# Optimization experiments

Measured on AMD Instinct MI355X. Metric: run time of the kernel, lower is better.

## Reference

```python
import jax, jax.numpy as jnp
import numpy as np
from jax.scipy.linalg import expm

N = 2048
B = 16384
S = 0.1  # Euler step size s


def _A_hat(Theta):
    # row-softmax of Theta
    A = jax.nn.softmax(Theta, axis=1)
    # zero_diag=True path: mask diagonal, renormalize rows (guard empty rows)
    mask = 1.0 - jnp.eye(N, dtype=Theta.dtype)
    A = A * mask
    rs = jnp.sum(A, axis=1, keepdims=True)
    rs = jnp.where(rs > 0, rs, jnp.ones_like(rs))
    return A / rs


def setup_inputs() -> dict:
    key = jax.random.key(0)
    k1, k2 = jax.random.split(key)
    x = jax.random.normal(k1, (B, N), dtype=jnp.float32)
    # kaiming_uniform_(a=0) on [N,N]: bound = sqrt(6 / N)
    bound = float(np.sqrt(6.0 / N))
    Theta = jax.random.uniform(k2, (N, N), dtype=jnp.float32, minval=-bound, maxval=bound)
    return {"x": x, "Theta": Theta}


def reference(x, Theta):
    A = _A_hat(Theta)
    L = jnp.eye(N, dtype=Theta.dtype) - A          # normalized Laplacian
    M = expm(-S * L)                               # scaling-and-squaring matrix exp
    return x @ M.T                                 # [B, N]
```

## Files before the change

### kernel.cpp

```cpp
#include <hip/hip_runtime.h>
#include <hip/hip_bf16.h>
#include <cstdint>
#include <cstddef>

typedef unsigned short u16;
typedef unsigned int u32;
typedef __attribute__((ext_vector_type(8))) short bf16x8;
typedef __attribute__((ext_vector_type(4))) float f32x4;

#define ND 2048
#define BD 16384

#define C0 0.9048374180359595f
#define C1 0.09048374180359595f
#define C2 0.004524187090179798f
#define C3 1.5080623633932658e-4f
#define C4 3.770155908483165e-6f

__device__ __forceinline__ u16 f2bf(float f) {
  union { float f; u32 u; } v; v.f = f;
  u32 x = v.u;
  return (u16)((x + 0x7fffu + ((x >> 16) & 1u)) >> 16);
}

__device__ __forceinline__ float bf2f(u16 b) {
  union { u32 u; float f; } v; v.u = ((u32)b) << 16; return v.f;
}

__device__ __forceinline__ void cp16(const void* g, void* l) {
  __builtin_amdgcn_global_load_lds(
      (const __attribute__((address_space(1))) u32*)g,
      (__attribute__((address_space(3))) u32*)l, 16, 0, 0);
}

__global__ void cvt_x(const float* __restrict__ in, u16* __restrict__ out) {
  const size_t i = ((size_t)blockIdx.x * 256 + threadIdx.x) * 8;
  float4 a = ((const float4*)(in + i))[0];
  float4 b = ((const float4*)(in + i))[1];
  union { u16 u[8]; uint4 v; } o;
  o.u[0] = f2bf(a.x); o.u[1] = f2bf(a.y); o.u[2] = f2bf(a.z); o.u[3] = f2bf(a.w);
  o.u[4] = f2bf(b.x); o.u[5] = f2bf(b.y); o.u[6] = f2bf(b.z); o.u[7] = f2bf(b.w);
  *((uint4*)(out + i)) = o.v;
}

__global__ void row_softmax(const float* __restrict__ Theta, u16* __restrict__ Abf) {
  const int row = blockIdx.x;
  const int t = threadIdx.x;
  const float* tr = Theta + (size_t)row * ND;
  const int j0 = t * 8;
  float4 v0 = ((const float4*)tr)[t * 2];
  float4 v1 = ((const float4*)tr)[t * 2 + 1];
  float vals[8] = {v0.x, v0.y, v0.z, v0.w, v1.x, v1.y, v1.z, v1.w};

  float mx = -1e30f;
#pragma unroll
  for (int j = 0; j < 8; ++j)
    if (j0 + j != row) mx = fmaxf(mx, vals[j]);
#pragma unroll
  for (int o = 32; o > 0; o >>= 1) mx = fmaxf(mx, __shfl_xor(mx, o, 64));

  __shared__ float redm[4], reds[4];
  const int wv = t >> 6, ln = t & 63;
  if (ln == 0) redm[wv] = mx;
  __syncthreads();
  mx = fmaxf(fmaxf(redm[0], redm[1]), fmaxf(redm[2], redm[3]));

  float e[8];
  float s = 0.f;
#pragma unroll
  for (int j = 0; j < 8; ++j) {
    e[j] = (j0 + j == row) ? 0.f : expf(vals[j] - mx);
    s += e[j];
  }
#pragma unroll
  for (int o = 32; o > 0; o >>= 1) s += __shfl_xor(s, o, 64);
  if (ln == 0) reds[wv] = s;
  __syncthreads();
  s = reds[0] + reds[1] + reds[2] + reds[3];
  const float inv = 1.0f / s;

  union { u16 u[8]; uint4 v; } ab;
#pragma unroll
  for (int j = 0; j < 8; ++j) ab.u[j] = f2bf(e[j] * inv);
  *((uint4*)(Abf + (size_t)row * ND + j0)) = ab.v;
}

__global__ void transpose_bf16(const u16* __restrict__ in, u16* __restrict__ out) {
  __shared__ u16 tile[64][65];
  const int bx = blockIdx.x & 31, by = blockIdx.x >> 5;
  const int x = threadIdx.x & 63, y0 = threadIdx.x >> 6;
#pragma unroll
  for (int yy = y0; yy < 64; yy += 4)
    tile[yy][x] = in[(size_t)(by * 64 + yy) * ND + bx * 64 + x];
  __syncthreads();
#pragma unroll
  for (int yy = y0; yy < 64; yy += 4)
    out[(size_t)(bx * 64 + yy) * ND + by * 64 + x] = tile[x][yy];
}

template <int BM, int BN, int WM, int WN, int THREADS, int MODE>
__global__ __launch_bounds__(THREADS, 2) void gemm_deep(
    const u16* __restrict__ Ag, const u16* __restrict__ Bg,
    float* __restrict__ Fo, u16* __restrict__ Bo, u16* __restrict__ Bo2,
    const u16* __restrict__ Aux, const float* __restrict__ Xf,
    int Nn, int K, int gridn) {
  constexpr int LOGM = (BM == 256) ? 8 : 7;
  constexpr int LOGN = (BN == 256) ? 8 : 7;
  constexpr int FM = BM / WM / 16;
  constexpr int FN = BN / WN / 16;
  constexpr int CHA = BM * 4 / THREADS;
  constexpr int CHB = BN * 4 / THREADS;

  __shared__ u16 lA[3][BM * 32];
  __shared__ u16 lB[3][BN * 32];

  const int tid = threadIdx.x;
  const int lane = tid & 63;
  const int wave = tid >> 6;
  const int wm = wave / WN;
  const int wn = wave % WN;
  const int lr = lane & 15;
  const int kc = lane >> 4;

  const int nwg = gridDim.x;
  const int bid = blockIdx.x;
  const int swz = (bid & 7) * (nwg >> 3) + (bid >> 3);
  const int bm = swz / gridn;
  const int bn = swz % gridn;

  const u16* Abase = Ag + (size_t)bm * BM * K;
  const u16* Bbase = Bg + (size_t)bn * BN * K;

  f32x4 acc[FM][FN];
#pragma unroll
  for (int i = 0; i < FM; ++i)
#pragma unroll
    for (int j = 0; j < FN; ++j)
      acc[i][j] = (f32x4){0.f, 0.f, 0.f, 0.f};

  auto stage = [&](int s, int kt) {
    const int kbase = kt * 32;
#pragma unroll
    for (int q = 0; q < CHA; ++q) {
      int c = q * THREADS + tid;
      int kcc = c >> LOGM, row = c & (BM - 1);
      cp16(Abase + (size_t)row * K + kbase + kcc * 8, &lA[s][c * 8]);
    }
#pragma unroll
    for (int q = 0; q < CHB; ++q) {
      int c = q * THREADS + tid;
      int kcc = c >> LOGN, col = c & (BN - 1);
      cp16(Bbase + (size_t)col * K + kbase + kcc * 8, &lB[s][c * 8]);
    }
  };

  auto compute = [&](int s) {
    bf16x8 af[FM], bg[FN];
#pragma unroll
    for (int m = 0; m < FM; ++m) {
      int row = wm * (BM / WM) + m * 16 + lr;
      af[m] = *(const bf16x8*)&lA[s][(kc * BM + row) * 8];
    }
#pragma unroll
    for (int n = 0; n < FN; ++n) {
      int col = wn * (BN / WN) + n * 16 + lr;
      bg[n] = *(const bf16x8*)&lB[s][(kc * BN + col) * 8];
    }
    __builtin_amdgcn_s_setprio(1);
#pragma unroll
    for (int m = 0; m < FM; ++m)
#pragma unroll
      for (int n = 0; n < FN; ++n)
        acc[m][n] = __builtin_amdgcn_mfma_f32_16x16x32_bf16(af[m], bg[n], acc[m][n], 0, 0, 0);
    __builtin_amdgcn_s_setprio(0);
  };

  const int NT = K >> 5;
  stage(0, 0);
  stage(1, 1);
  for (int t = 0; t < NT - 2; ++t) {
    stage((t + 2) % 3, t + 2);
    asm volatile("s_waitcnt vmcnt(8)" ::: "memory");
    __builtin_amdgcn_s_barrier();
    compute(t % 3);
    __builtin_amdgcn_s_barrier();
  }
  asm volatile("s_waitcnt vmcnt(4)" ::: "memory");
  __builtin_amdgcn_s_barrier();
  compute((NT - 2) % 3);
  __builtin_amdgcn_s_barrier();
  asm volatile("s_waitcnt vmcnt(0)" ::: "memory");
  __builtin_amdgcn_s_barrier();
  compute((NT - 1) % 3);

  const int r0 = (lane >> 4) << 2;
#pragma unroll
  for (int m = 0; m < FM; ++m) {
    const int grow0 = bm * BM + wm * (BM / WM) + m * 16 + r0;
#pragma unroll
    for (int n = 0; n < FN; ++n) {
      const int gcol = bn * BN + wn * (BN / WN) + n * 16 + lr;
#pragma unroll
      for (int r = 0; r < 4; ++r) {
        const int grow = grow0 + r;
        const size_t idx = (size_t)grow * Nn + gcol;
        const float v = acc[m][n][r];
        if (MODE == 3) {
          Bo[idx] = f2bf(v);
          float tv = ((grow == gcol) ? C2 : 0.0f) + C3 * bf2f(Aux[idx]) + C4 * v;
          Bo2[idx] = f2bf(tv);
        } else if (MODE == 1) {
          Bo[idx] = f2bf(C1 * bf2f(Aux[idx]) + v);
        } else {
          Fo[idx] = C0 * Xf[idx] + v;
        }
      }
    }
  }
}

extern "C" void kernel_launch(void* const* d_in, const int* in_sizes, int n_in,
                              void* d_out, int out_size, void* d_ws, size_t ws_size,
                              hipStream_t stream) {
  const float* x = (const float*)d_in[0];
  const float* Theta = (const float*)d_in[1];
  float* out = (float*)d_out;

  char* ws = (char*)d_ws;
  u16* xbf  = (u16*)(ws);
  u16* Abf  = (u16*)(ws + 67108864);
  u16* Atbf = (u16*)(ws + 75497472);
  u16* P2   = (u16*)(ws + 83886080);
  u16* Tbf  = (u16*)(ws + 92274688);
  u16* Ttbf = (u16*)(ws + 100663296);
  u16* Rbf  = (u16*)(ws + 109051904);

  cvt_x<<<dim3(16384), dim3(256), 0, stream>>>(x, xbf);
  row_softmax<<<dim3(2048), dim3(256), 0, stream>>>(Theta, Abf);
  transpose_bf16<<<dim3(1024), dim3(256), 0, stream>>>(Abf, Atbf);
  gemm_deep<128, 128, 2, 2, 256, 3><<<dim3(256), dim3(256), 0, stream>>>(
      Abf, Atbf, nullptr, P2, Tbf, Abf, nullptr, ND, ND, 16);
  transpose_bf16<<<dim3(1024), dim3(256), 0, stream>>>(Tbf, Ttbf);
  gemm_deep<128, 128, 2, 2, 256, 1><<<dim3(256), dim3(256), 0, stream>>>(
      P2, Ttbf, nullptr, Rbf, nullptr, Abf, nullptr, ND, ND, 16);
  gemm_deep<256, 256, 2, 4, 512, 2><<<dim3(512), dim3(512), 0, stream>>>(
      xbf, Rbf, out, nullptr, nullptr, nullptr, x, ND, ND, 8);
}
```

Baseline: 635.6 us.

## Rewrite GEMM as half-tile ping-pong pipeline with BK=64 double buffering

Replaces the three-stage BK=32 GEMM with a double-buffered BK=64 kernel. Each block tile is split into four quadrant sub-tiles, and their LDS reads, MFMAs and next-tile prefetches are interleaved with barriers between them. The small 2048x2048 GEMMs switch from 128x128 tiles on 256 blocks to 64x64 tiles with 128 threads on 1024 blocks, to fill more compute units. Tile mapping changes to column-major block order (swz % gridm). The intent is better overlap of global loads with MFMA and higher occupancy, at the cost of more barriers and a more fragile hand-counted vmcnt schedule.

```diff
diff --git a/kernel.cpp b/kernel.cpp
--- a/kernel.cpp
+++ b/kernel.cpp
@@ -99,124 +99,148 @@
 }
 
 template <int BM, int BN, int WM, int WN, int THREADS, int MODE>
-__global__ __launch_bounds__(THREADS, 2) void gemm_deep(
+__global__ __launch_bounds__(THREADS, 2) void gemm8(
     const u16* __restrict__ Ag, const u16* __restrict__ Bg,
     float* __restrict__ Fo, u16* __restrict__ Bo, u16* __restrict__ Bo2,
     const u16* __restrict__ Aux, const float* __restrict__ Xf,
-    int Nn, int K, int gridn) {
-  constexpr int LOGM = (BM == 256) ? 8 : 7;
-  constexpr int LOGN = (BN == 256) ? 8 : 7;
-  constexpr int FM = BM / WM / 16;
-  constexpr int FN = BN / WN / 16;
-  constexpr int CHA = BM * 4 / THREADS;
-  constexpr int CHB = BN * 4 / THREADS;
-
-  __shared__ u16 lA[3][BM * 32];
-  __shared__ u16 lB[3][BN * 32];
+    int Nn, int K, int gridm) {
+  constexpr int BK = 64;
+  constexpr int HM = BM / 2, HN = BN / 2;
+  constexpr int RH = HM / WM, CH = HN / WN;
+  constexpr int FMH = RH / 16, FNH = CH / 16;
+  constexpr int LA = HM * 8 / THREADS;
+  constexpr int LB = HN * 8 / THREADS;
+  static_assert(LA == 2 && LB == 2, "vmcnt(4) math assumes 2+2 loads per half-pair");
+  static_assert(FMH >= 1 && FNH >= 1, "bad wave geometry");
+
+  __shared__ u16 lA[2][2][HM * BK];
+  __shared__ u16 lB[2][2][HN * BK];
 
   const int tid = threadIdx.x;
   const int lane = tid & 63;
   const int wave = tid >> 6;
-  const int wm = wave / WN;
-  const int wn = wave % WN;
-  const int lr = lane & 15;
-  const int kc = lane >> 4;
-
-  const int nwg = gridDim.x;
-  const int bid = blockIdx.x;
+  const int wm = wave / WN, wn = wave % WN;
+  const int lr = lane & 15, khi = lane >> 4;
+
+  const int nwg = gridDim.x, bid = blockIdx.x;
   const int swz = (bid & 7) * (nwg >> 3) + (bid >> 3);
-  const int bm = swz / gridn;
-  const int bn = swz % gridn;
-
-  const u16* Abase = Ag + (size_t)bm * BM * K;
-  const u16* Bbase = Bg + (size_t)bn * BN * K;
-
-  f32x4 acc[FM][FN];
-#pragma unroll
-  for (int i = 0; i < FM; ++i)
-#pragma unroll
-    for (int j = 0; j < FN; ++j)
+  const int bm = swz % gridm, bn = swz / gridm;
+
+  const u16* Ab = Ag + (size_t)bm * BM * K;
+  const u16* Bb = Bg + (size_t)bn * BN * K;
+
+  f32x4 acc[2 * FMH][2 * FNH];
+#pragma unroll
+  for (int i = 0; i < 2 * FMH; ++i)
+#pragma unroll
+    for (int j = 0; j < 2 * FNH; ++j)
       acc[i][j] = (f32x4){0.f, 0.f, 0.f, 0.f};
 
-  auto stage = [&](int s, int kt) {
-    const int kbase = kt * 32;
-#pragma unroll
-    for (int q = 0; q < CHA; ++q) {
+  auto stA = [&](int b, int h, int kt) {
+#pragma unroll
+    for (int q = 0; q < LA; ++q) {
       int c = q * THREADS + tid;
-      int kcc = c >> LOGM, row = c & (BM - 1);
-      cp16(Abase + (size_t)row * K + kbase + kcc * 8, &lA[s][c * 8]);
+      int kc = c / HM, row = c % HM;
+      cp16(Ab + (size_t)(h * HM + row) * K + kt * BK + kc * 8, &lA[b][h][c * 8]);
     }
-#pragma unroll
-    for (int q = 0; q < CHB; ++q) {
+  };
+  auto stB = [&](int b, int h, int kt) {
+#pragma unroll
+    for (int q = 0; q < LB; ++q) {
       int c = q * THREADS + tid;
-      int kcc = c >> LOGN, col = c & (BN - 1);
-      cp16(Bbase + (size_t)col * K + kbase + kcc * 8, &lB[s][c * 8]);
+      int kc = c / HN, col = c % HN;
+      cp16(Bb + (size_t)(h * HN + col) * K + kt * BK + kc * 8, &lB[b][h][c * 8]);
     }
   };
 
-  auto compute = [&](int s) {
-    bf16x8 af[FM], bg[FN];
-#pragma unroll
-    for (int m = 0; m < FM; ++m) {
-      int row = wm * (BM / WM) + m * 16 + lr;
-      af[m] = *(const bf16x8*)&lA[s][(kc * BM + row) * 8];
-    }
-#pragma unroll
-    for (int n = 0; n < FN; ++n) {
-      int col = wn * (BN / WN) + n * 16 + lr;
-      bg[n] = *(const bf16x8*)&lB[s][(kc * BN + col) * 8];
-    }
+  bf16x8 af[FMH][2], bfr[FNH][2];
+  auto rdA = [&](int b, int mh) {
+#pragma unroll
+    for (int fm = 0; fm < FMH; ++fm)
+#pragma unroll
+      for (int ks = 0; ks < 2; ++ks) {
+        int row = wm * RH + fm * 16 + lr;
+        int kc = ks * 4 + khi;
+        af[fm][ks] = *(const bf16x8*)&lA[b][mh][(kc * HM + row) * 8];
+      }
+  };
+  auto rdB = [&](int b, int nh) {
+#pragma unroll
+    for (int fn = 0; fn < FNH; ++fn)
+#pragma unroll
+      for (int ks = 0; ks < 2; ++ks) {
+        int col = wn * CH + fn * 16 + lr;
+        int kc = ks * 4 + khi;
+        bfr[fn][ks] = *(const bf16x8*)&lB[b][nh][(kc * HN + col) * 8];
+      }
+  };
+  auto mm = [&](int mh, int nh) {
     __builtin_amdgcn_s_setprio(1);
 #pragma unroll
-    for (int m = 0; m < FM; ++m)
-#pragma unroll
-      for (int n = 0; n < FN; ++n)
-        acc[m][n] = __builtin_amdgcn_mfma_f32_16x16x32_bf16(af[m], bg[n], acc[m][n], 0, 0, 0);
+    for (int ks = 0; ks < 2; ++ks)
+#pragma unroll
+      for (int fm = 0; fm < FMH; ++fm)
+#pragma unroll
+        for (int fn = 0; fn < FNH; ++fn)
+          acc[mh * FMH + fm][nh * FNH + fn] = __builtin_amdgcn_mfma_f32_16x16x32_bf16(
+              af[fm][ks], bfr[fn][ks], acc[mh * FMH + fm][nh * FNH + fn], 0, 0, 0);
     __builtin_amdgcn_s_setprio(0);
   };
 
-  const int NT = K >> 5;
-  stage(0, 0);
-  stage(1, 1);
-  for (int t = 0; t < NT - 2; ++t) {
-    stage((t + 2) % 3, t + 2);
-    asm volatile("s_waitcnt vmcnt(8)" ::: "memory");
-    __builtin_amdgcn_s_barrier();
-    compute(t % 3);
-    __builtin_amdgcn_s_barrier();
-  }
+  const int NT = K / BK;
+  stA(0, 0, 0); stB(0, 0, 0); stB(0, 1, 0); stA(0, 1, 0);
   asm volatile("s_waitcnt vmcnt(4)" ::: "memory");
   __builtin_amdgcn_s_barrier();
-  compute((NT - 2) % 3);
-  __builtin_amdgcn_s_barrier();
-  asm volatile("s_waitcnt vmcnt(0)" ::: "memory");
-  __builtin_amdgcn_s_barrier();
-  compute((NT - 1) % 3);
-
-  const int r0 = (lane >> 4) << 2;
-#pragma unroll
-  for (int m = 0; m < FM; ++m) {
-    const int grow0 = bm * BM + wm * (BM / WM) + m * 16 + r0;
-#pragma unroll
-    for (int n = 0; n < FN; ++n) {
-      const int gcol = bn * BN + wn * (BN / WN) + n * 16 + lr;
-#pragma unroll
-      for (int r = 0; r < 4; ++r) {
-        const int grow = grow0 + r;
-        const size_t idx = (size_t)grow * Nn + gcol;
-        const float v = acc[m][n][r];
-        if (MODE == 3) {
-          Bo[idx] = f2bf(v);
-          float tv = ((grow == gcol) ? C2 : 0.0f) + C3 * bf2f(Aux[idx]) + C4 * v;
-          Bo2[idx] = f2bf(tv);
-        } else if (MODE == 1) {
-          Bo[idx] = f2bf(C1 * bf2f(Aux[idx]) + v);
-        } else {
-          Fo[idx] = C0 * Xf[idx] + v;
+
+  for (int t = 0; t < NT; ++t) {
+    const int b = t & 1, nb = b ^ 1;
+    const bool pre = (t + 1 < NT);
+    rdA(b, 0); rdB(b, 0);
+    if (pre) { stA(nb, 0, t + 1); stB(nb, 0, t + 1); }
+    mm(0, 0);
+    if (pre) asm volatile("s_waitcnt vmcnt(4)" ::: "memory");
+    else     asm volatile("s_waitcnt vmcnt(0)" ::: "memory");
+    __builtin_amdgcn_s_barrier();
+    rdB(b, 1);
+    if (pre) { stB(nb, 1, t + 1); stA(nb, 1, t + 1); }
+    mm(0, 1);
+    __builtin_amdgcn_s_barrier();
+    rdA(b, 1);
+    mm(1, 1);
+    __builtin_amdgcn_s_barrier();
+    rdB(b, 0);
+    mm(1, 0);
+    if (pre) asm volatile("s_waitcnt vmcnt(4)" ::: "memory");
+    __builtin_amdgcn_s_barrier();
+  }
+
+#pragma unroll
+  for (int mh = 0; mh < 2; ++mh)
+#pragma unroll
+    for (int fm = 0; fm < FMH; ++fm) {
+      const int grow0 = bm * BM + mh * HM + wm * RH + fm * 16 + (khi << 2);
+#pragma unroll
+      for (int nh = 0; nh < 2; ++nh)
+#pragma unroll
+        for (int fn = 0; fn < FNH; ++fn) {
+          const int gcol = bn * BN + nh * HN + wn * CH + fn * 16 + lr;
+#pragma unroll
+          for (int r = 0; r < 4; ++r) {
+            const int grow = grow0 + r;
+            const size_t idx = (size_t)grow * Nn + gcol;
+            const float v = acc[mh * FMH + fm][nh * FNH + fn][r];
+            if (MODE == 3) {
+              Bo[idx] = f2bf(v);
+              float tv = ((grow == gcol) ? C2 : 0.0f) + C3 * bf2f(Aux[idx]) + C4 * v;
+              Bo2[idx] = f2bf(tv);
+            } else if (MODE == 1) {
+              Bo[idx] = f2bf(C1 * bf2f(Aux[idx]) + v);
+            } else {
+              Fo[idx] = C0 * Xf[idx] + v;
+            }
+          }
         }
-      }
     }
-  }
 }
 
 extern "C" void kernel_launch(void* const* d_in, const int* in_sizes, int n_in,
@@ -238,11 +262,11 @@
   cvt_x<<<dim3(16384), dim3(256), 0, stream>>>(x, xbf);
   row_softmax<<<dim3(2048), dim3(256), 0, stream>>>(Theta, Abf);
   transpose_bf16<<<dim3(1024), dim3(256), 0, stream>>>(Abf, Atbf);
-  gemm_deep<128, 128, 2, 2, 256, 3><<<dim3(256), dim3(256), 0, stream>>>(
-      Abf, Atbf, nullptr, P2, Tbf, Abf, nullptr, ND, ND, 16);
+  gemm8<64, 64, 1, 2, 128, 3><<<dim3(1024), dim3(128), 0, stream>>>(
+      Abf, Atbf, nullptr, P2, Tbf, Abf, nullptr, ND, ND, 32);
   transpose_bf16<<<dim3(1024), dim3(256), 0, stream>>>(Tbf, Ttbf);
-  gemm_deep<128, 128, 2, 2, 256, 1><<<dim3(256), dim3(256), 0, stream>>>(
-      P2, Ttbf, nullptr, Rbf, nullptr, Abf, nullptr, ND, ND, 16);
-  gemm_deep<256, 256, 2, 4, 512, 2><<<dim3(512), dim3(512), 0, stream>>>(
-      xbf, Rbf, out, nullptr, nullptr, nullptr, x, ND, ND, 8);
-}
+  gemm8<64, 64, 1, 2, 128, 1><<<dim3(1024), dim3(128), 0, stream>>>(
+      P2, Ttbf, nullptr, Rbf, nullptr, Abf, nullptr, ND, ND, 32);
+  gemm8<256, 256, 2, 4, 512, 2><<<dim3(512), dim3(512), 0, stream>>>(
+      xbf, Rbf, out, nullptr, nullptr, nullptr, x, ND, ND, 64);
+}
```

Result: faster. 586.6 us (-7.7%).
